# Optimization experiments

Hardware: AMD Instinct MI355X
Metric: run time of the kernel (lower is better)

The kernel has to match this reference:

```python
import jax, jax.numpy as jnp
import numpy as np
from jax import lax

IOU_THRESHOLD = 0.1
B, N = 4, 8192


def setup_inputs() -> dict:
    key = jax.random.key(0)
    # [B, 5, N]: rows 0..3 = cx, cy, w, h; row 4 = confidence score in (0, 1)
    outputs = jax.random.uniform(key, (B, 5, N), dtype=jnp.float32)
    return {"outputs": outputs}


def _nms_single(p):
    """Greedy NMS on one image. p: [5, N] -> [5, N] with kept boxes
    compacted to the front (original column order preserved) and the rest
    zero-padded. Matches the torch loop: repeatedly take the highest-scoring
    surviving box, drop all boxes with IoU >= threshold (box keeps itself),
    and drop boxes with score <= 0."""
    boxes, scores = p[:4], p[4]
    n = scores.shape[0]
    order = jnp.argsort(-scores)            # descending score order
    b = boxes[:, order]

    x1 = b[0] - b[2] * 0.5
    y1 = b[1] - b[3] * 0.5
    x2 = b[0] + b[2] * 0.5
    y2 = b[1] + b[3] * 0.5
    area = (x2 - x1) * (y2 - y1)

    iw = jnp.clip(jnp.minimum(x2[:, None], x2[None, :]) - jnp.maximum(x1[:, None], x1[None, :]), 0.0)
    ih = jnp.clip(jnp.minimum(y2[:, None], y2[None, :]) - jnp.maximum(y1[:, None], y1[None, :]), 0.0)
    inter = iw * ih
    union = area[:, None] + area[None, :] - inter
    iou = inter / (union + 1e-8)            # [N, N] in sorted order

    idx_range = jnp.arange(n)
    keep_init = scores[order] > 0           # non_zero_scores filter

    def body(i, keep):
        # if box i (in score order) survives, suppress j with IoU >= thr, j != i
        row_keep = (iou[i] < IOU_THRESHOLD) | (idx_range == i)
        return jnp.where(keep[i], keep & row_keep, keep)

    keep_sorted = lax.fori_loop(0, n, body, keep_init)

    # map keep mask back to original column order
    keep_orig = jnp.zeros((n,), bool).at[order].set(keep_sorted)
    # stable compaction: kept columns first, original relative order preserved
    perm = jnp.argsort(jnp.where(keep_orig, 0, 1), stable=True)
    gathered = p[:, perm]                    # [5, N]
    valid = idx_range < jnp.sum(keep_orig)
    return jnp.where(valid[None, :], gathered, 0.0)


def reference(outputs):
    # torch version pads to the max detections across the batch; here we keep
    # the fixed width N (extra columns are zero), same kept values/order.
    return jax.vmap(_nms_single)(outputs)


if __name__ == "__main__":
    inp = setup_inputs()
    out = jax.jit(reference)(**inp)
    print(out.shape, out.dtype)
```

## Files before the change

kernel.cpp:

```cpp
#include <hip/hip_runtime.h>

#pragma clang fp contract(off)

#define NBOX 8192
#define BLK  1024
#define EPT  8
#define NBUCK 2048
#define NB 256
#define IOU_THR 0.1f

typedef unsigned short u16;
typedef unsigned int u32;
typedef unsigned long long u64;

#define MND 0x1.999999p-4

#define SMEM_TOT 161408

__global__ __launch_bounds__(BLK, 4) void nms_kernel(const float* __restrict__ in,
                                                     float* __restrict__ out) {
    __shared__ __align__(16) char smem[SMEM_TOT];
    const int img = blockIdx.x;
    const float* __restrict__ p = in + (size_t)img * 5 * NBOX;
    float* __restrict__ o = out + (size_t)img * 5 * NBOX;
    const int t = threadIdx.x;
    const int lane = t & 63;
    const int wid = t >> 6;

    float4* box   = (float4*)smem;
    u16* A        = (u16*)(smem + 131072);
    float4* bx    = (float4*)(smem + 147456);
    u64 (*mat)[4] = (u64(*)[4])(smem + 151552);
    u32* pfxA     = (u32*)(smem + 151552);
    u32* kom      = (u32*)(smem + 159744);
    int* wcnt     = (int*)(smem + 160768);
    u64* keptQ    = (u64*)(smem + 160832);
    int* S0sh     = (int*)(smem + 160864);
    u16* kidx     = (u16*)(smem + 160872);
    u64* skey  = (u64*)smem;
    u32* hist  = (u32*)(smem + 65536);
    u32* bbase = (u32*)(smem + 73728);

    {
        float4 z; z.x = z.y = z.z = z.w = 0.0f;
        float4* o4 = (float4*)o;
#pragma unroll
        for (int e = 0; e < 10; e++) o4[t + e * BLK] = z;
    }

    for (int i = t; i < NBUCK; i += BLK) hist[i] = 0;
    if (t < 256) kom[t] = 0;
    if (t == 0) *S0sh = 0;
    __syncthreads();

    u32 mybkt[EPT], myarr[EPT], mykeyhi[EPT];
#pragma unroll
    for (int e = 0; e < EPT; e++) {
        int j = t + e * BLK;
        float s = p[4 * NBOX + j];
        u32 u = __float_as_uint(s);
        u32 ordb = u ^ (u32)(((int)u >> 31) | (int)0x80000000);
        mykeyhi[e] = ~ordb;
        int vb = (int)(s * (float)NBUCK);
        vb = vb < 0 ? 0 : (vb > NBUCK - 1 ? NBUCK - 1 : vb);
        mybkt[e] = (u32)(NBUCK - 1 - vb);
        myarr[e] = atomicAdd(&hist[mybkt[e]], 1u);
        u64 bal = __ballot(s > 0.0f);
        if (lane == 0) atomicAdd(S0sh, (int)__popcll(bal));
    }
    __syncthreads();

    {
        u32 h0 = hist[2 * t], h1 = hist[2 * t + 1];
        int v = (int)(h0 + h1);
        int x = v;
        for (int d = 1; d < 64; d <<= 1) {
            int y = __shfl_up(x, d, 64);
            if (lane >= d) x += y;
        }
        if (lane == 63) wcnt[wid] = x;
        __syncthreads();
        int wb = 0;
        for (int i = 0; i < wid; i++) wb += wcnt[i];
        int excl = wb + x - v;
        bbase[2 * t] = (u32)excl;
        bbase[2 * t + 1] = (u32)excl + h0;
    }
    __syncthreads();

#pragma unroll
    for (int e = 0; e < EPT; e++) {
        u32 pos = bbase[mybkt[e]] + myarr[e];
        skey[pos] = ((u64)mykeyhi[e] << 32) | (u32)(t + e * BLK);
    }
    __syncthreads();

#pragma unroll
    for (int e = 0; e < EPT; e++) {
        u32 b = mybkt[e];
        u32 lo = bbase[b], hi2 = lo + hist[b];
        u64 me = ((u64)mykeyhi[e] << 32) | (u32)(t + e * BLK);
        u32 r = lo;
        for (u32 q = lo; q < hi2; q++) r += (skey[q] < me) ? 1u : 0u;
        A[r] = (u16)(t + e * BLK);
    }
    __syncthreads();
    int S = *S0sh;

#pragma unroll
    for (int e = 0; e < EPT; e++) {
        int j = t + e * BLK;
        float cx = p[j], cy = p[NBOX + j];
        float w_ = p[2 * NBOX + j], h_ = p[3 * NBOX + j];
        box[j] = make_float4(cx - w_ * 0.5f, cy - h_ * 0.5f,
                             cx + w_ * 0.5f, cy + h_ * 0.5f);
    }
    __syncthreads();

    if (t < NB) bx[t] = box[A[t]];
    ((u64*)mat)[t] = 0;
    __syncthreads();

    while (S > 0) {
        int nb = S < NB ? S : NB;

        {
            int i = t >> 2, q = t & 3;
            if (i > 0 && i < nb) {
                int clo = (i * q) >> 2;
                int chi = (i * (q + 1)) >> 2;
                if (chi > clo) {
                    float4 bi = bx[i];
                    float ari = (bi.z - bi.x) * (bi.w - bi.y);
                    u64 acc = 0;
                    for (int c = clo; c < chi; c++) {
                        float4 bc = bx[c];
                        float arc = (bc.z - bc.x) * (bc.w - bc.y);
                        float iw = fmaxf(fminf(bi.z, bc.z) - fmaxf(bi.x, bc.x), 0.0f);
                        float ih = fmaxf(fminf(bi.w, bc.w) - fmaxf(bi.y, bc.y), 0.0f);
                        float inter = iw * ih;
                        float t2 = (ari + arc) - inter;
                        float uu = t2 + 1e-8f;
                        if ((double)inter > MND * (double)uu) acc |= (1ull << (c - clo));
                    }
                    if (acc) {
                        int w0 = clo >> 6, sh = clo & 63;
                        atomicOr(&mat[i][w0], acc << sh);
                        if (sh && (((chi - 1) >> 6) != w0))
                            atomicOr(&mat[i][w0 + 1], acc >> (64 - sh));
                    }
                }
            }
        }
        __syncthreads();

        if (wid == 0) {
            u64 r0[4], r1[4], r2[4], r3[4];
#pragma unroll
            for (int wq = 0; wq < 4; wq++) {
                r0[wq] = mat[lane][wq];
                r1[wq] = mat[64 + lane][wq];
                r2[wq] = mat[128 + lane][wq];
                r3[wq] = mat[192 + lane][wq];
            }
            u64 A0, A1, A2, A3;
            {
                int n0 = nb;       A0 = n0 <= 0 ? 0ull : (n0 >= 64 ? ~0ull : ((1ull << n0) - 1ull));
                int n1 = nb - 64;  A1 = n1 <= 0 ? 0ull : (n1 >= 64 ? ~0ull : ((1ull << n1) - 1ull));
                int n2 = nb - 128; A2 = n2 <= 0 ? 0ull : (n2 >= 64 ? ~0ull : ((1ull << n2) - 1ull));
                int n3 = nb - 192; A3 = n3 <= 0 ? 0ull : (n3 >= 64 ? ~0ull : ((1ull << n3) - 1ull));
            }
            u64 K0 = 0, K1 = 0, K2 = 0, K3 = 0;
            u64 lm = (1ull << lane) - 1ull;
            while (A0 | A1 | A2 | A3) {
                bool c0b = ((A0 >> lane) & 1) && !(r0[0] & A0 & lm);
                bool c1b = ((A1 >> lane) & 1) && !((r1[0] & A0) | (r1[1] & A1 & lm));
                bool c2b = ((A2 >> lane) & 1) && !((r2[0] & A0) | (r2[1] & A1) | (r2[2] & A2 & lm));
                bool c3b = ((A3 >> lane) & 1) && !((r3[0] & A0) | (r3[1] & A1) | (r3[2] & A2) | (r3[3] & A3 & lm));
                u64 C0 = __ballot(c0b), C1 = __ballot(c1b), C2 = __ballot(c2b), C3 = __ballot(c3b);
                K0 |= C0; K1 |= C1; K2 |= C2; K3 |= C3;
                A0 &= ~C0; A1 &= ~C1; A2 &= ~C2; A3 &= ~C3;
                bool s0b = ((A0 >> lane) & 1) && ((r0[0] & C0) | (r0[1] & C1) | (r0[2] & C2) | (r0[3] & C3));
                bool s1b = ((A1 >> lane) & 1) && ((r1[0] & C0) | (r1[1] & C1) | (r1[2] & C2) | (r1[3] & C3));
                bool s2b = ((A2 >> lane) & 1) && ((r2[0] & C0) | (r2[1] & C1) | (r2[2] & C2) | (r2[3] & C3));
                bool s3b = ((A3 >> lane) & 1) && ((r3[0] & C0) | (r3[1] & C1) | (r3[2] & C2) | (r3[3] & C3));
                A0 &= ~__ballot(s0b); A1 &= ~__ballot(s1b); A2 &= ~__ballot(s2b); A3 &= ~__ballot(s3b);
            }
            if (lane < 4) keptQ[lane] = lane == 0 ? K0 : lane == 1 ? K1 : lane == 2 ? K2 : K3;
        }
        __syncthreads();

        ((u64*)mat)[t] = 0;
        u64 kq0 = keptQ[0], kq1 = keptQ[1], kq2 = keptQ[2], kq3 = keptQ[3];
        int nk = (int)(__popcll(kq0) + __popcll(kq1) + __popcll(kq2) + __popcll(kq3));
        if (t < nb) {
            int wq = t >> 6;
            u64 kq = wq == 0 ? kq0 : wq == 1 ? kq1 : wq == 2 ? kq2 : kq3;
            if ((kq >> (t & 63)) & 1) {
                int j = (int)A[t];
                atomicOr(&kom[j >> 5], 1u << (j & 31));
                int pk = 0;
                if (wq > 0) pk += (int)__popcll(kq0);
                if (wq > 1) pk += (int)__popcll(kq1);
                if (wq > 2) pk += (int)__popcll(kq2);
                pk += (int)__popcll(kq & ((1ull << (t & 63)) - 1ull));
                kidx[pk] = (u16)t;
            }
        }
        int tailN = S - nb;
        int C = (tailN + BLK - 1) / BLK;
        int st = nb + t * C;
        int en = st + C; if (en > S) en = S;
        float4 eb[EPT]; float ea[EPT]; u16 ei[EPT];
        u32 am = 0;
#pragma unroll
        for (int e = 0; e < EPT; e++) {
            int pos = st + e;
            if (e < C && pos < en) {
                u16 j = A[pos];
                ei[e] = j;
                float4 b = box[j];
                eb[e] = b;
                ea[e] = (b.z - b.x) * (b.w - b.y);
                am |= (1u << e);
            }
        }
        __syncthreads();

        if (am) {
            for (int c = 0; c < nk; c++) {
                float4 cb = bx[kidx[c]];
                float arc = (cb.z - cb.x) * (cb.w - cb.y);
#pragma unroll
                for (int e = 0; e < EPT; e++) {
                    if (am & (1u << e)) {
                        float iw = fminf(eb[e].z, cb.z) - fmaxf(eb[e].x, cb.x);
                        float ih = fminf(eb[e].w, cb.w) - fmaxf(eb[e].y, cb.y);
                        if (iw > 0.0f && ih > 0.0f) {
                            float inter = iw * ih;
                            float t2 = (ea[e] + arc) - inter;
                            float uu = t2 + 1e-8f;
                            if ((double)inter > MND * (double)uu) am &= ~(1u << e);
                        }
                    }
                }
                if (!am) break;
            }
        }

        {
            int cnt = __popc(am);
            int x = cnt;
            for (int d = 1; d < 64; d <<= 1) {
                int y = __shfl_up(x, d, 64);
                if (lane >= d) x += y;
            }
            if (lane == 63) wcnt[wid] = x;
            __syncthreads();
            int wb = 0, tot = 0;
            for (int i = 0; i < BLK / 64; i++) {
                int v = wcnt[i];
                if (i < wid) wb += v;
                tot += v;
            }
            int off = wb + x - cnt;
#pragma unroll
            for (int e = 0; e < EPT; e++) {
                if (am & (1u << e)) {
                    A[off] = ei[e];
                    if (off < NB) bx[off] = eb[e];
                    off++;
                }
            }
            __syncthreads();
            S = tot;
        }
    }
    __syncthreads();

    {
        u32 w = (t < 256) ? kom[t] : 0u;
        int c = __popc(w);
        int x = c;
        for (int d = 1; d < 64; d <<= 1) {
            int y = __shfl_up(x, d, 64);
            if (lane >= d) x += y;
        }
        if (lane == 63) wcnt[wid] = x;
        __syncthreads();
        int wb = 0;
        for (int i = 0; i < wid; i++) wb += wcnt[i];
        if (t < 256) pfxA[t] = (u32)(wb + x - c);
    }
    __syncthreads();
    for (int j = t; j < NBOX; j += BLK) {
        u32 km = kom[j >> 5];
        if ((km >> (j & 31)) & 1u) {
            int pos = (int)(pfxA[j >> 5] + (u32)__popc(km & ((1u << (j & 31)) - 1u)));
            o[0 * NBOX + pos] = p[0 * NBOX + j];
            o[1 * NBOX + pos] = p[1 * NBOX + j];
            o[2 * NBOX + pos] = p[2 * NBOX + j];
            o[3 * NBOX + pos] = p[3 * NBOX + j];
            o[4 * NBOX + pos] = p[4 * NBOX + j];
        }
    }
}

extern "C" void kernel_launch(void* const* d_in, const int* in_sizes, int n_in,
                              void* d_out, int out_size, void* d_ws, size_t ws_size,
                              hipStream_t stream) {
    const float* in = (const float*)d_in[0];
    float* out = (float*)d_out;
    int B = in_sizes[0] / (5 * NBOX);
    hipLaunchKernelGGL(nms_kernel, dim3(B), dim3(BLK), 0, stream, in, out);
}
```

Measured before the change: 158.8 us.

## Overlap tail box loading with wave-0 greedy resolve and stage kept boxes

```diff
diff --git a/kernel.cpp b/kernel.cpp
--- a/kernel.cpp
+++ b/kernel.cpp
@@ -31,12 +31,12 @@
     u16* A        = (u16*)(smem + 131072);
     float4* bx    = (float4*)(smem + 147456);
     u64 (*mat)[4] = (u64(*)[4])(smem + 151552);
+    float4* kx    = (float4*)(smem + 155648);
     u32* pfxA     = (u32*)(smem + 151552);
     u32* kom      = (u32*)(smem + 159744);
     int* wcnt     = (int*)(smem + 160768);
     u64* keptQ    = (u64*)(smem + 160832);
     int* S0sh     = (int*)(smem + 160864);
-    u16* kidx     = (u16*)(smem + 160872);
     u64* skey  = (u64*)smem;
     u32* hist  = (u32*)(smem + 65536);
     u32* bbase = (u32*)(smem + 73728);
@@ -154,6 +154,15 @@
         }
         __syncthreads();
 
+        int tailN = S - nb;
+        int C1 = 0, base0 = nb;
+        if (tailN > 0) {
+            int lim = tailN < 7680 ? tailN : 7680;
+            C1 = (lim + 959) / 960;
+            base0 = nb + 960 * C1;
+        }
+        float4 eb[EPT]; float ea[EPT]; u16 ei[EPT];
+        u32 am = 0;
         if (wid == 0) {
             u64 r0[4], r1[4], r2[4], r3[4];
 #pragma unroll
@@ -177,20 +186,35 @@
                 bool c1b = ((A1 >> lane) & 1) && !((r1[0] & A0) | (r1[1] & A1 & lm));
                 bool c2b = ((A2 >> lane) & 1) && !((r2[0] & A0) | (r2[1] & A1) | (r2[2] & A2 & lm));
                 bool c3b = ((A3 >> lane) & 1) && !((r3[0] & A0) | (r3[1] & A1) | (r3[2] & A2) | (r3[3] & A3 & lm));
-                u64 C0 = __ballot(c0b), C1 = __ballot(c1b), C2 = __ballot(c2b), C3 = __ballot(c3b);
-                K0 |= C0; K1 |= C1; K2 |= C2; K3 |= C3;
-                A0 &= ~C0; A1 &= ~C1; A2 &= ~C2; A3 &= ~C3;
-                bool s0b = ((A0 >> lane) & 1) && ((r0[0] & C0) | (r0[1] & C1) | (r0[2] & C2) | (r0[3] & C3));
-                bool s1b = ((A1 >> lane) & 1) && ((r1[0] & C0) | (r1[1] & C1) | (r1[2] & C2) | (r1[3] & C3));
-                bool s2b = ((A2 >> lane) & 1) && ((r2[0] & C0) | (r2[1] & C1) | (r2[2] & C2) | (r2[3] & C3));
-                bool s3b = ((A3 >> lane) & 1) && ((r3[0] & C0) | (r3[1] & C1) | (r3[2] & C2) | (r3[3] & C3));
+                u64 C0_ = __ballot(c0b), C1_ = __ballot(c1b), C2_ = __ballot(c2b), C3_ = __ballot(c3b);
+                K0 |= C0_; K1 |= C1_; K2 |= C2_; K3 |= C3_;
+                A0 &= ~C0_; A1 &= ~C1_; A2 &= ~C2_; A3 &= ~C3_;
+                bool s0b = ((A0 >> lane) & 1) && ((r0[0] & C0_) | (r0[1] & C1_) | (r0[2] & C2_) | (r0[3] & C3_));
+                bool s1b = ((A1 >> lane) & 1) && ((r1[0] & C0_) | (r1[1] & C1_) | (r1[2] & C2_) | (r1[3] & C3_));
+                bool s2b = ((A2 >> lane) & 1) && ((r2[0] & C0_) | (r2[1] & C1_) | (r2[2] & C2_) | (r2[3] & C3_));
+                bool s3b = ((A3 >> lane) & 1) && ((r3[0] & C0_) | (r3[1] & C1_) | (r3[2] & C2_) | (r3[3] & C3_));
                 A0 &= ~__ballot(s0b); A1 &= ~__ballot(s1b); A2 &= ~__ballot(s2b); A3 &= ~__ballot(s3b);
             }
             if (lane < 4) keptQ[lane] = lane == 0 ? K0 : lane == 1 ? K1 : lane == 2 ? K2 : K3;
-        }
-        __syncthreads();
-
-        ((u64*)mat)[t] = 0;
+        } else {
+            int ti = t - 64;
+            int st = nb + ti * C1;
+#pragma unroll
+            for (int e = 0; e < EPT; e++) {
+                int pos = st + e;
+                if (e < C1 && pos < S) {
+                    u16 j = A[pos];
+                    ei[e] = j;
+                    float4 b = box[j];
+                    eb[e] = b;
+                    ea[e] = (b.z - b.x) * (b.w - b.y);
+                    am |= (1u << e);
+                }
+            }
+        }
+        __syncthreads();
+
+        if (t < 512) ((u64*)mat)[t] = 0;
         u64 kq0 = keptQ[0], kq1 = keptQ[1], kq2 = keptQ[2], kq3 = keptQ[3];
         int nk = (int)(__popcll(kq0) + __popcll(kq1) + __popcll(kq2) + __popcll(kq3));
         if (t < nb) {
@@ -204,32 +228,30 @@
                 if (wq > 1) pk += (int)__popcll(kq1);
                 if (wq > 2) pk += (int)__popcll(kq2);
                 pk += (int)__popcll(kq & ((1ull << (t & 63)) - 1ull));
-                kidx[pk] = (u16)t;
-            }
-        }
-        int tailN = S - nb;
-        int C = (tailN + BLK - 1) / BLK;
-        int st = nb + t * C;
-        int en = st + C; if (en > S) en = S;
-        float4 eb[EPT]; float ea[EPT]; u16 ei[EPT];
-        u32 am = 0;
-#pragma unroll
-        for (int e = 0; e < EPT; e++) {
-            int pos = st + e;
-            if (e < C && pos < en) {
-                u16 j = A[pos];
-                ei[e] = j;
-                float4 b = box[j];
-                eb[e] = b;
-                ea[e] = (b.z - b.x) * (b.w - b.y);
-                am |= (1u << e);
+                kx[pk] = bx[t];
+            }
+        }
+        if (wid == 0 && base0 < S) {
+            int C0 = (S - base0 + 63) >> 6;
+            int st0 = base0 + lane * C0;
+#pragma unroll
+            for (int e = 0; e < EPT; e++) {
+                int pos = st0 + e;
+                if (e < C0 && pos < S) {
+                    u16 j = A[pos];
+                    ei[e] = j;
+                    float4 b = box[j];
+                    eb[e] = b;
+                    ea[e] = (b.z - b.x) * (b.w - b.y);
+                    am |= (1u << e);
+                }
             }
         }
         __syncthreads();
 
         if (am) {
             for (int c = 0; c < nk; c++) {
-                float4 cb = bx[kidx[c]];
+                float4 cb = kx[c];
                 float arc = (cb.z - cb.x) * (cb.w - cb.y);
 #pragma unroll
                 for (int e = 0; e < EPT; e++) {
@@ -258,10 +280,11 @@
             if (lane == 63) wcnt[wid] = x;
             __syncthreads();
             int wb = 0, tot = 0;
-            for (int i = 0; i < BLK / 64; i++) {
-                int v = wcnt[i];
-                if (i < wid) wb += v;
-                tot += v;
+            for (int i = 0; i < 16; i++) tot += wcnt[i];
+            if (wid == 0) {
+                for (int i = 1; i < 16; i++) wb += wcnt[i];
+            } else {
+                for (int i = 1; i < wid; i++) wb += wcnt[i];
             }
             int off = wb + x - cnt;
 #pragma unroll
@@ -272,6 +295,7 @@
                     off++;
                 }
             }
+            if (t >= 512) ((u64*)mat)[t] = 0;
             __syncthreads();
             S = tot;
         }
```

Measured after the change: 153.6 us. 3.3% less time.
